# Performance work log

Measured on AMD Instinct MI355X. Metric: run time of the kernel, lower is better.

The kernel has to match this reference:

```python
import jax, jax.numpy as jnp
import numpy as np

N_NODES = 25000
N_EDGES = 400000
IN_FEATS = 256
HIDDEN = 64
HEADS = 8
CLASSES = 32


def setup_inputs() -> dict:
    key = jax.random.key(0)
    ks = jax.random.split(key, 12)
    h = jax.random.normal(ks[0], (N_NODES, IN_FEATS), dtype=jnp.float32)
    src = jax.random.randint(ks[1], (N_EDGES,), 0, N_NODES, dtype=jnp.int32)
    dst = jnp.sort(jax.random.randint(ks[2], (N_EDGES,), 0, N_NODES, dtype=jnp.int32))
    s = 0.05  # param scale
    W1 = jax.random.normal(ks[3], (HIDDEN * HEADS, IN_FEATS), dtype=jnp.float32) * s
    al1 = jax.random.normal(ks[4], (1, HEADS, HIDDEN), dtype=jnp.float32) * s
    ar1 = jax.random.normal(ks[5], (1, HEADS, HIDDEN), dtype=jnp.float32) * s
    W2 = jax.random.normal(ks[6], (HIDDEN * HEADS, HIDDEN * HEADS), dtype=jnp.float32) * s
    al2 = jax.random.normal(ks[7], (1, HEADS, HIDDEN), dtype=jnp.float32) * s
    ar2 = jax.random.normal(ks[8], (1, HEADS, HIDDEN), dtype=jnp.float32) * s
    W3 = jax.random.normal(ks[9], (CLASSES, HIDDEN * HEADS), dtype=jnp.float32) * s
    al3 = jax.random.normal(ks[10], (1, 1, CLASSES), dtype=jnp.float32) * s
    ar3 = jax.random.normal(ks[11], (1, 1, CLASSES), dtype=jnp.float32) * s
    return dict(h=h, src=src, dst=dst, W1=W1, al1=al1, ar1=ar1,
                W2=W2, al2=al2, ar2=ar2, W3=W3, al3=al3, ar3=ar3)


def gat_layer(x, src, dst, W, al, ar, use_elu):
    # x: [N, Din]; W: [H*F, Din]; al/ar: [1, H, F]
    n = x.shape[0]
    H, F = al.shape[1], al.shape[2]
    z = (x @ W.T).reshape(n, H, F)                      # [N,H,F]
    el = jnp.sum(z * al, axis=-1)                       # [N,H]
    er = jnp.sum(z * ar, axis=-1)                       # [N,H]
    e = jax.nn.leaky_relu(el[src] + er[dst], 0.2)       # [E,H]
    # segment softmax over incoming edges of each dst node
    m = jax.ops.segment_max(e, dst, num_segments=n, indices_are_sorted=True)   # [N,H]
    ex = jnp.exp(e - m[dst])                            # [E,H]
    den = jax.ops.segment_sum(ex, dst, num_segments=n, indices_are_sorted=True)  # [N,H]
    alpha = ex / den[dst]                               # [E,H]
    out = jax.ops.segment_sum(alpha[:, :, None] * z[src], dst,
                              num_segments=n, indices_are_sorted=True)  # [N,H,F]
    if use_elu:
        out = jax.nn.elu(out)
    return out.reshape(n, H * F)


def reference(h, src, dst, W1, al1, ar1, W2, al2, ar2, W3, al3, ar3):
    x = gat_layer(h, src, dst, W1, al1, ar1, True)
    x = gat_layer(x, src, dst, W2, al2, ar2, True)
    x = gat_layer(x, src, dst, W3, al3, ar3, False)
    return x
```

## Files before the change

kernel.cpp:

```cpp
#include <hip/hip_runtime.h>
#include <cstdint>

#define DEVINL __device__ __forceinline__

typedef uint16_t u16;
typedef uint32_t u32;
typedef uint64_t u64;
typedef __attribute__((ext_vector_type(8))) short short8;
typedef __attribute__((ext_vector_type(4))) float floatx4;
typedef __attribute__((ext_vector_type(4))) u32 u32x4;
typedef const __attribute__((address_space(1))) void* gas_ptr;
typedef __attribute__((address_space(3))) void* las_ptr;

DEVINL u16 f2bf(float f) {
  u32 u = __float_as_uint(f);
  u32 r = u + 0x7FFFu + ((u >> 16) & 1u);
  return (u16)(r >> 16);
}
DEVINL float bf2f(u16 b) { return __uint_as_float((u32)b << 16); }
DEVINL float bf_lo(u32 u) { return __uint_as_float(u << 16); }
DEVINL float bf_hi(u32 u) { return __uint_as_float(u & 0xFFFF0000u); }


__global__ void rowstart_kernel(const int* __restrict__ dst, int* __restrict__ rs,
                                int N, int E) {
  int n = blockIdx.x * blockDim.x + threadIdx.x;
  if (n > N) return;
  int lo = 0, hi = E;
  while (lo < hi) { int mid = (lo + hi) >> 1; if (dst[mid] < n) lo = mid + 1; else hi = mid; }
  rs[n] = lo;
}

__global__ void zero3_kernel(float* __restrict__ z3, float* __restrict__ el,
                             float* __restrict__ er, int nz, int ne) {
  int i = blockIdx.x * blockDim.x + threadIdx.x;
  if (i < nz) { z3[i] = 0.f; return; }
  int j = i - nz;
  if (j < ne) { el[j] = 0.f; return; }
  j -= ne;
  if (j < ne) er[j] = 0.f;
}

__global__ __launch_bounds__(256)
void splitA_kernel(const float* __restrict__ in, u16* __restrict__ out,
                   int M, int Mpad) {
  int idx = blockIdx.x * blockDim.x + threadIdx.x;
  if (idx >= M * 256) return;
  int m = idx >> 8, k = idx & 255;
  float a = in[idx];
  u16 h = f2bf(a);
  u16 lo = f2bf(a - bf2f(h));
  size_t cs = (size_t)Mpad * 64;
  size_t pos = (size_t)m * 64 + (k & 63);
  out[(size_t)(k >> 6) * cs + pos] = h;
  out[(size_t)((k >> 6) + 4) * cs + pos] = lo;
}

__global__ __launch_bounds__(256)
void splitW_kernel(const float* __restrict__ W1, const float* __restrict__ W2,
                   const float* __restrict__ W3, u16* __restrict__ B1,
                   u16* __restrict__ B2, u16* __restrict__ B3) {
  int idx = blockIdx.x * blockDim.x + threadIdx.x;
  if (idx < 512 * 256) {
    int m = idx >> 8, k = idx & 255;
    u16 h = f2bf(W1[idx]);
    size_t cs = 512 * 64;
    size_t pos = (size_t)m * 64 + (k & 63);
    B1[(size_t)(k >> 6) * cs + pos] = h;
    B1[(size_t)((k >> 6) + 4) * cs + pos] = h;
    return;
  }
  idx -= 512 * 256;
  if (idx < 512 * 512) {
    int m = idx >> 9, k = idx & 511;
    u16 h = f2bf(W2[idx]);
    size_t cs = 512 * 64;
    size_t pos = (size_t)m * 64 + (k & 63);
    B2[(size_t)(k >> 6) * cs + pos] = h;
    B2[(size_t)((k >> 6) + 8) * cs + pos] = h;
    return;
  }
  idx -= 512 * 512;
  if (idx < 32 * 512) {
    int m = idx >> 9, k = idx & 511;
    u16 h = f2bf(W3[idx]);
    size_t cs = 32 * 64;
    size_t pos = (size_t)m * 64 + (k & 63);
    B3[(size_t)(k >> 6) * cs + pos] = h;
    B3[(size_t)((k >> 6) + 8) * cs + pos] = h;
  }
}

template<int BN, int OUTM>
__global__ __launch_bounds__(256)
void gemm_bt_kernel(const u16* __restrict__ A, const u16* __restrict__ B,
                    float* __restrict__ Cf, u16* __restrict__ Cb,
                    const float* __restrict__ al, const float* __restrict__ ar,
                    float* __restrict__ el, float* __restrict__ er,
                    int M, int Nout, int Mpad, int kcLen)
{
  constexpr int BM = 128, CF = BN / 16;
  constexpr int BCALLS_B = (BN * 64) / 512;
  __shared__ __align__(16) u16 As[2][BM * 64];
  __shared__ __align__(16) u16 Bs[2][BN * 64];
  const int tid  = threadIdx.x;
  const int wave = tid >> 6;
  const int lane = tid & 63;
  const int quad = lane >> 4;
  const int l16  = lane & 15;
  const int lrow = lane >> 3;
  const int lq   = lane & 7;

  int bx, by;
  if (OUTM == 1) {
    int bid = blockIdx.x;
    int nY = (M + 127) >> 7;
    int fullG = nY >> 3;
    if ((bid >> 5) < fullG) {
      int rem = bid & 31;
      by = ((bid >> 5) << 3) + (rem & 7);
      bx = rem >> 3;
    } else {
      int t = bid - (fullG << 5);
      int tailY = nY - (fullG << 3);
      by = (fullG << 3) + t % tailY;
      bx = t / tailY;
    }
  } else { bx = blockIdx.x; by = blockIdx.y; }

  const int rowBase = by * BM;
  const int colBase = (OUTM == 2) ? 0 : bx * BN;
  const int kcStart = (OUTM == 2) ? bx * kcLen : 0;

  floatx4 acc[2][CF];
  #pragma unroll
  for (int r = 0; r < 2; ++r)
    #pragma unroll
    for (int c = 0; c < CF; ++c)
      acc[r][c] = (floatx4){0.f, 0.f, 0.f, 0.f};

  const size_t aCS = (size_t)Mpad * 64;
  const size_t bCS = (size_t)Nout * 64;
  const u16* aTile = A + (size_t)rowBase * 64;
  const u16* bTile = B + (size_t)colBase * 64;

  auto stage = [&](int buf, int kc) {
    const u16* aB = aTile + (size_t)kc * aCS;
    #pragma unroll
    for (int i = 0; i < 4; ++i) {
      int c = wave * 4 + i;
      int row = c * 8 + lrow;
      const u16* gp = aB + row * 64 + ((lq ^ (row & 7)) << 3);
      __builtin_amdgcn_global_load_lds((gas_ptr)gp, (las_ptr)(&As[buf][c * 512]), 16, 0, 0);
    }
    const u16* bB = bTile + (size_t)kc * bCS;
    #pragma unroll
    for (int i = 0; i < BCALLS_B / 4; ++i) {
      int c = wave * (BCALLS_B / 4) + i;
      int row = c * 8 + lrow;
      const u16* gp = bB + row * 64 + ((lq ^ (row & 7)) << 3);
      __builtin_amdgcn_global_load_lds((gas_ptr)gp, (las_ptr)(&Bs[buf][c * 512]), 16, 0, 0);
    }
  };

  stage(0, kcStart);
  int cur = 0;
  for (int t = 0; t < kcLen; ++t) {
    __syncthreads();
    if (t + 1 < kcLen) stage(cur ^ 1, kcStart + t + 1);
    const u16* Asb = &As[cur][0];
    const u16* Bsb = &Bs[cur][0];
    #pragma unroll
    for (int kk = 0; kk < 2; ++kk) {
      const int r0 = 32 * wave + l16;
      const int r1 = r0 + 16;
      short8 a0 = *(const short8*)(Asb + r0 * 64 + ((((kk << 2) + quad) ^ (r0 & 7)) << 3));
      short8 a1 = *(const short8*)(Asb + r1 * 64 + ((((kk << 2) + quad) ^ (r1 & 7)) << 3));
      #pragma unroll
      for (int c = 0; c < CF; ++c) {
        int rb = 16 * c + l16;
        short8 b = *(const short8*)(Bsb + rb * 64 + ((((kk << 2) + quad) ^ (rb & 7)) << 3));
        acc[0][c] = __builtin_amdgcn_mfma_f32_16x16x32_bf16(a0, b, acc[0][c], 0, 0, 0);
        acc[1][c] = __builtin_amdgcn_mfma_f32_16x16x32_bf16(a1, b, acc[1][c], 0, 0, 0);
      }
    }
    cur ^= 1;
  }

  #pragma unroll
  for (int rt = 0; rt < 2; ++rt)
    #pragma unroll
    for (int c = 0; c < CF; ++c)
      #pragma unroll
      for (int i = 0; i < 4; ++i) {
        int gr = rowBase + 32 * wave + 16 * rt + quad * 4 + i;
        if (gr < M) {
          int gc = colBase + 16 * c + l16;
          if (OUTM == 1) Cb[(size_t)gr * Nout + gc] = f2bf(acc[rt][c][i]);
          else           atomicAdd(Cf + (size_t)gr * Nout + gc, acc[rt][c][i]);
        }
      }

  if (OUTM == 1) {
    #pragma unroll
    for (int rt = 0; rt < 2; ++rt)
      #pragma unroll
      for (int i = 0; i < 4; ++i) {
        int gr = rowBase + 32 * wave + 16 * rt + quad * 4 + i;
        #pragma unroll
        for (int hp = 0; hp < 2; ++hp) {
          float sl = 0.f, sr = 0.f;
          #pragma unroll
          for (int cc = 0; cc < 4; ++cc) {
            int c = hp * 4 + cc;
            int gc = colBase + 16 * c + l16;
            float zv = acc[rt][c][i];
            sl += zv * al[gc];
            sr += zv * ar[gc];
          }
          #pragma unroll
          for (int m = 1; m < 16; m <<= 1) {
            sl += __shfl_xor(sl, m, 64);
            sr += __shfl_xor(sr, m, 64);
          }
          if (l16 == 0 && gr < M) {
            int hh = colBase / 64 + hp;
            el[(size_t)gr * 8 + hh] = sl;
            er[(size_t)gr * 8 + hh] = sr;
          }
        }
      }
  } else {
    #pragma unroll
    for (int rt = 0; rt < 2; ++rt)
      #pragma unroll
      for (int i = 0; i < 4; ++i) {
        int gr = rowBase + 32 * wave + 16 * rt + quad * 4 + i;
        float sl = 0.f, sr = 0.f;
        #pragma unroll
        for (int c = 0; c < CF; ++c) {
          int gc = 16 * c + l16;
          float zv = acc[rt][c][i];
          sl += zv * al[gc];
          sr += zv * ar[gc];
        }
        #pragma unroll
        for (int m = 1; m < 16; m <<= 1) {
          sl += __shfl_xor(sl, m, 64);
          sr += __shfl_xor(sr, m, 64);
        }
        if (l16 == 0 && gr < M) {
          atomicAdd(el + gr, sl);
          atomicAdd(er + gr, sr);
        }
      }
  }
}

__global__ __launch_bounds__(64)
void agg_bf16_kernel(const u16* __restrict__ z, const float* __restrict__ el,
                     const float* __restrict__ er, const int* __restrict__ src,
                     const int* __restrict__ rs, u16* __restrict__ a2out, int Mpad)
{
  const int n = blockIdx.x, tid = threadIdx.x;
  const int s = rs[n], e = rs[n + 1];
  const int c0 = tid * 8;
  const int h = tid >> 3;
  const float er_h = er[(size_t)n * 8 + h];

  float acc[8];
  #pragma unroll
  for (int j = 0; j < 8; ++j) acc[j] = 0.f;
  float den = 0.f;

  for (int k0 = s; k0 < e; k0 += 8) {
    const int kc = e - k0;
    #pragma unroll
    for (int kk = 0; kk < 8; ++kk) {
      if (kk < kc) {
        int si = src[k0 + kk];
        float v = el[(size_t)si * 8 + h] + er_h;
        v = (v > 0.f) ? v : 0.2f * v;
        float wgt = __expf(v);
        u32x4 zz = *(const u32x4*)(z + (size_t)si * 512 + c0);
        #pragma unroll
        for (int j = 0; j < 4; ++j) {
          acc[2 * j]     += wgt * bf_lo(zz[j]);
          acc[2 * j + 1] += wgt * bf_hi(zz[j]);
        }
        den += wgt;
      }
    }
  }

  const float r = (e > s) ? (1.f / den) : 0.f;
  u32x4 hp, lp;
  #pragma unroll
  for (int j = 0; j < 4; ++j) {
    float o0 = acc[2 * j] * r, o1 = acc[2 * j + 1] * r;
    o0 = (o0 > 0.f) ? o0 : (__expf(o0) - 1.f);
    o1 = (o1 > 0.f) ? o1 : (__expf(o1) - 1.f);
    u16 h0 = f2bf(o0), h1 = f2bf(o1);
    u16 l0 = f2bf(o0 - bf2f(h0)), l1 = f2bf(o1 - bf2f(h1));
    hp[j] = ((u32)h1 << 16) | h0;
    lp[j] = ((u32)l1 << 16) | l0;
  }
  const int ck = tid >> 3;
  const int ko = (tid & 7) << 3;
  const size_t cs = (size_t)Mpad * 64;
  u16* p = a2out + (size_t)n * 64 + ko;
  *(u32x4*)(p + (size_t)ck * cs) = hp;
  *(u32x4*)(p + (size_t)(ck + 8) * cs) = lp;
}

__global__ __launch_bounds__(64)
void agg3_kernel(const float* __restrict__ z, const float* __restrict__ el,
                 const float* __restrict__ er, const int* __restrict__ src,
                 const int* __restrict__ rs, float* __restrict__ out)
{
  const int n = blockIdx.x, tid = threadIdx.x;
  const int s = rs[n], e = rs[n + 1];
  const bool active = (tid < 32);
  const float er_n = er[n];
  float acc = 0.f, den = 0.f;

  for (int k0 = s; k0 < e; k0 += 8) {
    const int kc = e - k0;
    #pragma unroll
    for (int kk = 0; kk < 8; ++kk) {
      if (kk < kc) {
        int si = src[k0 + kk];
        float v = el[si] + er_n;
        v = (v > 0.f) ? v : 0.2f * v;
        float wgt = __expf(v);
        if (active) acc += wgt * z[(size_t)si * 32 + tid];
        den += wgt;
      }
    }
  }
  if (active) out[(size_t)n * 32 + tid] = (e > s) ? (acc / den) : 0.f;
}

extern "C" void kernel_launch(void* const* d_in, const int* in_sizes, int n_in,
                              void* d_out, int out_size, void* d_ws, size_t ws_size,
                              hipStream_t stream)
{
  constexpr int N = 25000, E = 400000, K1 = 256, HF = 512, CLS = 32;
  constexpr int Mpad = 25088;
  const float* h   = (const float*)d_in[0];
  const int*   src = (const int*)d_in[1];
  const int*   dst = (const int*)d_in[2];
  const float* W1  = (const float*)d_in[3];
  const float* al1 = (const float*)d_in[4];
  const float* ar1 = (const float*)d_in[5];
  const float* W2  = (const float*)d_in[6];
  const float* al2 = (const float*)d_in[7];
  const float* ar2 = (const float*)d_in[8];
  const float* W3  = (const float*)d_in[9];
  const float* al3 = (const float*)d_in[10];
  const float* ar3 = (const float*)d_in[11];
  float* out = (float*)d_out;

  char* w = (char*)d_ws;
  auto take = [&](size_t bytes) {
    char* p = w;
    w += (bytes + 255) & ~(size_t)255;
    return p;
  };
  int*   rs = (int*)  take((size_t)(N + 1) * sizeof(int));
  float* el = (float*)take((size_t)N * 8 * sizeof(float));
  float* er = (float*)take((size_t)N * 8 * sizeof(float));
  float* z3 = (float*)take((size_t)N * CLS * sizeof(float));
  u16*   zb = (u16*)  take((size_t)N * HF * sizeof(u16));
  u16*   A2 = (u16*)  take((size_t)16 * Mpad * 64 * sizeof(u16));
  u16*   B1 = (u16*)  take((size_t)8  * HF * 64 * sizeof(u16));
  u16*   B2 = (u16*)  take((size_t)16 * HF * 64 * sizeof(u16));
  u16*   B3 = (u16*)  take((size_t)16 * CLS * 64 * sizeof(u16));
  u16*   A1 = A2;

  rowstart_kernel<<<dim3((N + 1 + 255) / 256), 256, 0, stream>>>(dst, rs, N, E);
  splitA_kernel<<<dim3((N * K1) / 256), 256, 0, stream>>>(h, A1, N, Mpad);
  splitW_kernel<<<dim3(1600), 256, 0, stream>>>(W1, W2, W3, B1, B2, B3);

  const int gemmBlocks = 4 * (Mpad / 128);

  gemm_bt_kernel<128, 1><<<dim3(gemmBlocks), 256, 0, stream>>>(A1, B1, nullptr, zb,
      al1, ar1, el, er, N, HF, Mpad, 8);
  agg_bf16_kernel<<<dim3(N), 64, 0, stream>>>(zb, el, er, src, rs, A2, Mpad);

  gemm_bt_kernel<128, 1><<<dim3(gemmBlocks), 256, 0, stream>>>(A2, B2, nullptr, zb,
      al2, ar2, el, er, N, HF, Mpad, 16);
  agg_bf16_kernel<<<dim3(N), 64, 0, stream>>>(zb, el, er, src, rs, A2, Mpad);

  zero3_kernel<<<dim3((N * CLS + 2 * N + 255) / 256), 256, 0, stream>>>(z3, el, er, N * CLS, N);
  gemm_bt_kernel<32, 2><<<dim3(4, Mpad / 128), 256, 0, stream>>>(A2, B3, z3, nullptr,
      al3, ar3, el, er, N, CLS, Mpad, 4);
  agg3_kernel<<<dim3(N), 64, 0, stream>>>(z3, el, er, src, rs, out);
}
```

Measured before the change: 374.8 us.

## Fuse prep kernels, use 512-thread GEMM blocks, replace el/er atomics with partials

Merges the rowstart, splitA, splitW and zero-fill kernels into one prep launch, removing several small launches. The GEMM now runs 8 waves of 16 rows each instead of 4 waves of 32 rows, which halves per-wave accumulator registers and spreads the global-to-LDS staging over more waves. In the split-K layer-3 GEMM, the el/er atomic adds are replaced by per-split partial buffers that agg3 sums, so el/er no longer need zeroing. The cost is less A-fragment reuse per wave in the GEMM and four extra el loads per edge in agg3.

```diff
diff --git a/kernel.cpp b/kernel.cpp
--- a/kernel.cpp
+++ b/kernel.cpp
@@ -22,77 +22,75 @@
 DEVINL float bf_hi(u32 u) { return __uint_as_float(u & 0xFFFF0000u); }
 
 
-__global__ void rowstart_kernel(const int* __restrict__ dst, int* __restrict__ rs,
-                                int N, int E) {
-  int n = blockIdx.x * blockDim.x + threadIdx.x;
-  if (n > N) return;
-  int lo = 0, hi = E;
-  while (lo < hi) { int mid = (lo + hi) >> 1; if (dst[mid] < n) lo = mid + 1; else hi = mid; }
-  rs[n] = lo;
-}
-
-__global__ void zero3_kernel(float* __restrict__ z3, float* __restrict__ el,
-                             float* __restrict__ er, int nz, int ne) {
-  int i = blockIdx.x * blockDim.x + threadIdx.x;
-  if (i < nz) { z3[i] = 0.f; return; }
-  int j = i - nz;
-  if (j < ne) { el[j] = 0.f; return; }
-  j -= ne;
-  if (j < ne) er[j] = 0.f;
-}
-
 __global__ __launch_bounds__(256)
-void splitA_kernel(const float* __restrict__ in, u16* __restrict__ out,
-                   int M, int Mpad) {
-  int idx = blockIdx.x * blockDim.x + threadIdx.x;
-  if (idx >= M * 256) return;
-  int m = idx >> 8, k = idx & 255;
-  float a = in[idx];
-  u16 h = f2bf(a);
-  u16 lo = f2bf(a - bf2f(h));
-  size_t cs = (size_t)Mpad * 64;
-  size_t pos = (size_t)m * 64 + (k & 63);
-  out[(size_t)(k >> 6) * cs + pos] = h;
-  out[(size_t)((k >> 6) + 4) * cs + pos] = lo;
-}
-
-__global__ __launch_bounds__(256)
-void splitW_kernel(const float* __restrict__ W1, const float* __restrict__ W2,
-                   const float* __restrict__ W3, u16* __restrict__ B1,
-                   u16* __restrict__ B2, u16* __restrict__ B3) {
-  int idx = blockIdx.x * blockDim.x + threadIdx.x;
-  if (idx < 512 * 256) {
+void prep_kernel(const int* __restrict__ dst, int* __restrict__ rs,
+                 const float* __restrict__ h, u16* __restrict__ A1,
+                 const float* __restrict__ W1, const float* __restrict__ W2,
+                 const float* __restrict__ W3, u16* __restrict__ B1,
+                 u16* __restrict__ B2, u16* __restrict__ B3,
+                 float* __restrict__ z3, int N, int E, int Mpad)
+{
+  const int b = blockIdx.x, tid = threadIdx.x;
+  if (b < 25000) {
+    int idx = b * 256 + tid;
     int m = idx >> 8, k = idx & 255;
-    u16 h = f2bf(W1[idx]);
-    size_t cs = 512 * 64;
+    float a = h[idx];
+    u16 hi = f2bf(a);
+    u16 lo = f2bf(a - bf2f(hi));
+    size_t cs = (size_t)Mpad * 64;
     size_t pos = (size_t)m * 64 + (k & 63);
-    B1[(size_t)(k >> 6) * cs + pos] = h;
-    B1[(size_t)((k >> 6) + 4) * cs + pos] = h;
+    A1[(size_t)(k >> 6) * cs + pos] = hi;
+    A1[(size_t)((k >> 6) + 4) * cs + pos] = lo;
     return;
   }
-  idx -= 512 * 256;
-  if (idx < 512 * 512) {
-    int m = idx >> 9, k = idx & 511;
-    u16 h = f2bf(W2[idx]);
-    size_t cs = 512 * 64;
-    size_t pos = (size_t)m * 64 + (k & 63);
-    B2[(size_t)(k >> 6) * cs + pos] = h;
-    B2[(size_t)((k >> 6) + 8) * cs + pos] = h;
+  if (b < 26600) {
+    int idx = (b - 25000) * 256 + tid;
+    if (idx < 512 * 256) {
+      int m = idx >> 8, k = idx & 255;
+      u16 hh = f2bf(W1[idx]);
+      size_t cs = 512 * 64;
+      size_t pos = (size_t)m * 64 + (k & 63);
+      B1[(size_t)(k >> 6) * cs + pos] = hh;
+      B1[(size_t)((k >> 6) + 4) * cs + pos] = hh;
+      return;
+    }
+    idx -= 512 * 256;
+    if (idx < 512 * 512) {
+      int m = idx >> 9, k = idx & 511;
+      u16 hh = f2bf(W2[idx]);
+      size_t cs = 512 * 64;
+      size_t pos = (size_t)m * 64 + (k & 63);
+      B2[(size_t)(k >> 6) * cs + pos] = hh;
+      B2[(size_t)((k >> 6) + 8) * cs + pos] = hh;
+      return;
+    }
+    idx -= 512 * 512;
+    {
+      int m = idx >> 9, k = idx & 511;
+      u16 hh = f2bf(W3[idx]);
+      size_t cs = 32 * 64;
+      size_t pos = (size_t)m * 64 + (k & 63);
+      B3[(size_t)(k >> 6) * cs + pos] = hh;
+      B3[(size_t)((k >> 6) + 8) * cs + pos] = hh;
+      return;
+    }
+  }
+  if (b < 26698) {
+    int n = (b - 26600) * 256 + tid;
+    if (n > N) return;
+    int lo = 0, hi = E;
+    while (lo < hi) { int mid = (lo + hi) >> 1; if (dst[mid] < n) lo = mid + 1; else hi = mid; }
+    rs[n] = lo;
     return;
   }
-  idx -= 512 * 512;
-  if (idx < 32 * 512) {
-    int m = idx >> 9, k = idx & 511;
-    u16 h = f2bf(W3[idx]);
-    size_t cs = 32 * 64;
-    size_t pos = (size_t)m * 64 + (k & 63);
-    B3[(size_t)(k >> 6) * cs + pos] = h;
-    B3[(size_t)((k >> 6) + 8) * cs + pos] = h;
+  {
+    int i = (b - 26698) * 256 + tid;
+    if (i < N * 32) z3[i] = 0.f;
   }
 }
 
 template<int BN, int OUTM>
-__global__ __launch_bounds__(256)
+__global__ __launch_bounds__(512)
 void gemm_bt_kernel(const u16* __restrict__ A, const u16* __restrict__ B,
                     float* __restrict__ Cf, u16* __restrict__ Cb,
                     const float* __restrict__ al, const float* __restrict__ ar,
@@ -132,12 +130,10 @@
   const int colBase = (OUTM == 2) ? 0 : bx * BN;
   const int kcStart = (OUTM == 2) ? bx * kcLen : 0;
 
-  floatx4 acc[2][CF];
+  floatx4 acc[CF];
   #pragma unroll
-  for (int r = 0; r < 2; ++r)
-    #pragma unroll
-    for (int c = 0; c < CF; ++c)
-      acc[r][c] = (floatx4){0.f, 0.f, 0.f, 0.f};
+  for (int c = 0; c < CF; ++c)
+    acc[c] = (floatx4){0.f, 0.f, 0.f, 0.f};
 
   const size_t aCS = (size_t)Mpad * 64;
   const size_t bCS = (size_t)Nout * 64;
@@ -147,19 +143,21 @@
   auto stage = [&](int buf, int kc) {
     const u16* aB = aTile + (size_t)kc * aCS;
     #pragma unroll
-    for (int i = 0; i < 4; ++i) {
-      int c = wave * 4 + i;
+    for (int i = 0; i < 2; ++i) {
+      int c = wave + 8 * i;
       int row = c * 8 + lrow;
       const u16* gp = aB + row * 64 + ((lq ^ (row & 7)) << 3);
       __builtin_amdgcn_global_load_lds((gas_ptr)gp, (las_ptr)(&As[buf][c * 512]), 16, 0, 0);
     }
     const u16* bB = bTile + (size_t)kc * bCS;
     #pragma unroll
-    for (int i = 0; i < BCALLS_B / 4; ++i) {
-      int c = wave * (BCALLS_B / 4) + i;
-      int row = c * 8 + lrow;
-      const u16* gp = bB + row * 64 + ((lq ^ (row & 7)) << 3);
-      __builtin_amdgcn_global_load_lds((gas_ptr)gp, (las_ptr)(&Bs[buf][c * 512]), 16, 0, 0);
+    for (int i = 0; i < (BCALLS_B + 7) / 8; ++i) {
+      int c = wave + 8 * i;
+      if (c < BCALLS_B) {
+        int row = c * 8 + lrow;
+        const u16* gp = bB + row * 64 + ((lq ^ (row & 7)) << 3);
+        __builtin_amdgcn_global_load_lds((gas_ptr)gp, (las_ptr)(&Bs[buf][c * 512]), 16, 0, 0);
+      }
     }
   };
 
@@ -170,77 +168,44 @@
     if (t + 1 < kcLen) stage(cur ^ 1, kcStart + t + 1);
     const u16* Asb = &As[cur][0];
     const u16* Bsb = &Bs[cur][0];
+    const int r0 = 16 * wave + l16;
     #pragma unroll
     for (int kk = 0; kk < 2; ++kk) {
-      const int r0 = 32 * wave + l16;
-      const int r1 = r0 + 16;
       short8 a0 = *(const short8*)(Asb + r0 * 64 + ((((kk << 2) + quad) ^ (r0 & 7)) << 3));
-      short8 a1 = *(const short8*)(Asb + r1 * 64 + ((((kk << 2) + quad) ^ (r1 & 7)) << 3));
       #pragma unroll
       for (int c = 0; c < CF; ++c) {
         int rb = 16 * c + l16;
         short8 b = *(const short8*)(Bsb + rb * 64 + ((((kk << 2) + quad) ^ (rb & 7)) << 3));
-        acc[0][c] = __builtin_amdgcn_mfma_f32_16x16x32_bf16(a0, b, acc[0][c], 0, 0, 0);
-        acc[1][c] = __builtin_amdgcn_mfma_f32_16x16x32_bf16(a1, b, acc[1][c], 0, 0, 0);
+        acc[c] = __builtin_amdgcn_mfma_f32_16x16x32_bf16(a0, b, acc[c], 0, 0, 0);
       }
     }
     cur ^= 1;
   }
 
   #pragma unroll
-  for (int rt = 0; rt < 2; ++rt)
-    #pragma unroll
-    for (int c = 0; c < CF; ++c)
+  for (int c = 0; c < CF; ++c)
+    #pragma unroll
+    for (int i = 0; i < 4; ++i) {
+      int gr = rowBase + 16 * wave + quad * 4 + i;
+      if (gr < M) {
+        int gc = colBase + 16 * c + l16;
+        if (OUTM == 1) Cb[(size_t)gr * Nout + gc] = f2bf(acc[c][i]);
+        else           atomicAdd(Cf + (size_t)gr * Nout + gc, acc[c][i]);
+      }
+    }
+
+  if (OUTM == 1) {
+    #pragma unroll
+    for (int i = 0; i < 4; ++i) {
+      int gr = rowBase + 16 * wave + quad * 4 + i;
       #pragma unroll
-      for (int i = 0; i < 4; ++i) {
-        int gr = rowBase + 32 * wave + 16 * rt + quad * 4 + i;
-        if (gr < M) {
-          int gc = colBase + 16 * c + l16;
-          if (OUTM == 1) Cb[(size_t)gr * Nout + gc] = f2bf(acc[rt][c][i]);
-          else           atomicAdd(Cf + (size_t)gr * Nout + gc, acc[rt][c][i]);
-        }
-      }
-
-  if (OUTM == 1) {
-    #pragma unroll
-    for (int rt = 0; rt < 2; ++rt)
-      #pragma unroll
-      for (int i = 0; i < 4; ++i) {
-        int gr = rowBase + 32 * wave + 16 * rt + quad * 4 + i;
-        #pragma unroll
-        for (int hp = 0; hp < 2; ++hp) {
-          float sl = 0.f, sr = 0.f;
-          #pragma unroll
-          for (int cc = 0; cc < 4; ++cc) {
-            int c = hp * 4 + cc;
-            int gc = colBase + 16 * c + l16;
-            float zv = acc[rt][c][i];
-            sl += zv * al[gc];
-            sr += zv * ar[gc];
-          }
-          #pragma unroll
-          for (int m = 1; m < 16; m <<= 1) {
-            sl += __shfl_xor(sl, m, 64);
-            sr += __shfl_xor(sr, m, 64);
-          }
-          if (l16 == 0 && gr < M) {
-            int hh = colBase / 64 + hp;
-            el[(size_t)gr * 8 + hh] = sl;
-            er[(size_t)gr * 8 + hh] = sr;
-          }
-        }
-      }
-  } else {
-    #pragma unroll
-    for (int rt = 0; rt < 2; ++rt)
-      #pragma unroll
-      for (int i = 0; i < 4; ++i) {
-        int gr = rowBase + 32 * wave + 16 * rt + quad * 4 + i;
+      for (int hp = 0; hp < 2; ++hp) {
         float sl = 0.f, sr = 0.f;
         #pragma unroll
-        for (int c = 0; c < CF; ++c) {
-          int gc = 16 * c + l16;
-          float zv = acc[rt][c][i];
+        for (int cc = 0; cc < 4; ++cc) {
+          int c = hp * 4 + cc;
+          int gc = colBase + 16 * c + l16;
+          float zv = acc[c][i];
           sl += zv * al[gc];
           sr += zv * ar[gc];
         }
@@ -250,10 +215,34 @@
           sr += __shfl_xor(sr, m, 64);
         }
         if (l16 == 0 && gr < M) {
-          atomicAdd(el + gr, sl);
-          atomicAdd(er + gr, sr);
+          int hh = colBase / 64 + hp;
+          el[(size_t)gr * 8 + hh] = sl;
+          er[(size_t)gr * 8 + hh] = sr;
         }
       }
+    }
+  } else {
+    #pragma unroll
+    for (int i = 0; i < 4; ++i) {
+      int gr = rowBase + 16 * wave + quad * 4 + i;
+      float sl = 0.f, sr = 0.f;
+      #pragma unroll
+      for (int c = 0; c < CF; ++c) {
+        int gc = 16 * c + l16;
+        float zv = acc[c][i];
+        sl += zv * al[gc];
+        sr += zv * ar[gc];
+      }
+      #pragma unroll
+      for (int m = 1; m < 16; m <<= 1) {
+        sl += __shfl_xor(sl, m, 64);
+        sr += __shfl_xor(sr, m, 64);
+      }
+      if (l16 == 0 && gr < M) {
+        el[(size_t)bx * M + gr] = sl;
+        er[(size_t)bx * M + gr] = sr;
+      }
+    }
   }
 }
 
@@ -314,14 +303,14 @@
 }
 
 __global__ __launch_bounds__(64)
-void agg3_kernel(const float* __restrict__ z, const float* __restrict__ el,
-                 const float* __restrict__ er, const int* __restrict__ src,
-                 const int* __restrict__ rs, float* __restrict__ out)
+void agg3_kernel(const float* __restrict__ z, const float* __restrict__ elp,
+                 const float* __restrict__ erp, const int* __restrict__ src,
+                 const int* __restrict__ rs, float* __restrict__ out, int N)
 {
   const int n = blockIdx.x, tid = threadIdx.x;
   const int s = rs[n], e = rs[n + 1];
   const bool active = (tid < 32);
-  const float er_n = er[n];
+  const float er_n = erp[n] + erp[N + n] + erp[2 * N + n] + erp[3 * N + n];
   float acc = 0.f, den = 0.f;
 
   for (int k0 = s; k0 < e; k0 += 8) {
@@ -330,7 +319,8 @@
     for (int kk = 0; kk < 8; ++kk) {
       if (kk < kc) {
         int si = src[k0 + kk];
-        float v = el[si] + er_n;
+        float elv = elp[si] + elp[N + si] + elp[2 * N + si] + elp[3 * N + si];
+        float v = elv + er_n;
         v = (v > 0.f) ? v : 0.2f * v;
         float wgt = __expf(v);
         if (active) acc += wgt * z[(size_t)si * 32 + tid];
@@ -367,33 +357,33 @@
     w += (bytes + 255) & ~(size_t)255;
     return p;
   };
-  int*   rs = (int*)  take((size_t)(N + 1) * sizeof(int));
-  float* el = (float*)take((size_t)N * 8 * sizeof(float));
-  float* er = (float*)take((size_t)N * 8 * sizeof(float));
-  float* z3 = (float*)take((size_t)N * CLS * sizeof(float));
-  u16*   zb = (u16*)  take((size_t)N * HF * sizeof(u16));
-  u16*   A2 = (u16*)  take((size_t)16 * Mpad * 64 * sizeof(u16));
-  u16*   B1 = (u16*)  take((size_t)8  * HF * 64 * sizeof(u16));
-  u16*   B2 = (u16*)  take((size_t)16 * HF * 64 * sizeof(u16));
-  u16*   B3 = (u16*)  take((size_t)16 * CLS * 64 * sizeof(u16));
-  u16*   A1 = A2;
-
-  rowstart_kernel<<<dim3((N + 1 + 255) / 256), 256, 0, stream>>>(dst, rs, N, E);
-  splitA_kernel<<<dim3((N * K1) / 256), 256, 0, stream>>>(h, A1, N, Mpad);
-  splitW_kernel<<<dim3(1600), 256, 0, stream>>>(W1, W2, W3, B1, B2, B3);
+  int*   rs  = (int*)  take((size_t)(N + 1) * sizeof(int));
+  float* el  = (float*)take((size_t)N * 8 * sizeof(float));
+  float* er  = (float*)take((size_t)N * 8 * sizeof(float));
+  float* elp = (float*)take((size_t)4 * N * sizeof(float));
+  float* erp = (float*)take((size_t)4 * N * sizeof(float));
+  float* z3  = (float*)take((size_t)N * CLS * sizeof(float));
+  u16*   zb  = (u16*)  take((size_t)N * HF * sizeof(u16));
+  u16*   A2  = (u16*)  take((size_t)16 * Mpad * 64 * sizeof(u16));
+  u16*   B1  = (u16*)  take((size_t)8  * HF * 64 * sizeof(u16));
+  u16*   B2  = (u16*)  take((size_t)16 * HF * 64 * sizeof(u16));
+  u16*   B3  = (u16*)  take((size_t)16 * CLS * 64 * sizeof(u16));
+  u16*   A1  = A2;
+
+  prep_kernel<<<dim3(25000 + 1600 + 98 + 3125), 256, 0, stream>>>(
+      dst, rs, h, A1, W1, W2, W3, B1, B2, B3, z3, N, E, Mpad);
 
   const int gemmBlocks = 4 * (Mpad / 128);
 
-  gemm_bt_kernel<128, 1><<<dim3(gemmBlocks), 256, 0, stream>>>(A1, B1, nullptr, zb,
+  gemm_bt_kernel<128, 1><<<dim3(gemmBlocks), 512, 0, stream>>>(A1, B1, nullptr, zb,
       al1, ar1, el, er, N, HF, Mpad, 8);
   agg_bf16_kernel<<<dim3(N), 64, 0, stream>>>(zb, el, er, src, rs, A2, Mpad);
 
-  gemm_bt_kernel<128, 1><<<dim3(gemmBlocks), 256, 0, stream>>>(A2, B2, nullptr, zb,
+  gemm_bt_kernel<128, 1><<<dim3(gemmBlocks), 512, 0, stream>>>(A2, B2, nullptr, zb,
       al2, ar2, el, er, N, HF, Mpad, 16);
   agg_bf16_kernel<<<dim3(N), 64, 0, stream>>>(zb, el, er, src, rs, A2, Mpad);
 
-  zero3_kernel<<<dim3((N * CLS + 2 * N + 255) / 256), 256, 0, stream>>>(z3, el, er, N * CLS, N);
-  gemm_bt_kernel<32, 2><<<dim3(4, Mpad / 128), 256, 0, stream>>>(A2, B3, z3, nullptr,
-      al3, ar3, el, er, N, CLS, Mpad, 4);
-  agg3_kernel<<<dim3(N), 64, 0, stream>>>(z3, el, er, src, rs, out);
-}
+  gemm_bt_kernel<32, 2><<<dim3(4, Mpad / 128), 512, 0, stream>>>(A2, B3, z3, nullptr,
+      al3, ar3, elp, erp, N, CLS, Mpad, 4);
+  agg3_kernel<<<dim3(N), 64, 0, stream>>>(z3, elp, erp, src, rs, out, N);
+}
```

After: 370.3 us. No clear change (-1.2%).
